# Performance work log

Measured on AMD Instinct MI355X. Metric: run time of the kernel, lower is better.

Reference implementation:

```python
import jax, jax.numpy as jnp
import numpy as np

BATCH = 4096  # number of rows in the sparse input matrix (static for segment_sum)


def setup_inputs() -> dict:
    key = jax.random.key(0)
    k1, k2, k3, k4 = jax.random.split(key, 4)
    nnz = 262144
    in_features, out_features = 32000, 256
    row_idx = jnp.sort(jax.random.randint(k1, (nnz,), 0, BATCH, dtype=jnp.int32))
    col_idx = jax.random.randint(k2, (nnz,), 0, in_features, dtype=jnp.int32)
    vals = jax.random.uniform(k3, (nnz,), dtype=jnp.float32)
    weight = jax.random.normal(k4, (in_features, out_features), dtype=jnp.float32) / np.sqrt(out_features)
    bias = jnp.zeros((out_features,), dtype=jnp.float32)
    return {"row_idx": row_idx, "col_idx": col_idx, "vals": vals,
            "weight": weight, "bias": bias}


def reference(row_idx, col_idx, vals, weight, bias):
    # out = sparse_input @ weight + bias
    # sparse_input is COO: (row_idx, col_idx, vals), shape [BATCH, in_features]
    # gather weight rows for each nonzero, scale by value, sum per output row
    contrib = vals[:, None] * weight[col_idx]          # [nnz, out_features]
    out = jax.ops.segment_sum(contrib, row_idx, num_segments=BATCH)  # [BATCH, out]
    return out + bias
```

## Files before the change

kernel.cpp:

```cpp
#include <hip/hip_runtime.h>


constexpr int BATCH = 4096;
constexpr int ROWS_PER_BLOCK = 4;

__global__ __launch_bounds__(256, 4) void sparse_linear_kernel(
    const int*   __restrict__ row_idx,
    const int*   __restrict__ col_idx,
    const float* __restrict__ vals,
    const float* __restrict__ weight,
    const float* __restrict__ bias,
    float*       __restrict__ out,
    int nnz)
{
    const int wave = threadIdx.x >> 6;
    const int lane = threadIdx.x & 63;
    const int r    = blockIdx.x * ROWS_PER_BLOCK + wave;

    int lo = 0, hi = nnz;
    while (lo < hi) {
        int mid = (lo + hi) >> 1;
        if (row_idx[mid] < r) lo = mid + 1; else hi = mid;
    }
    const int start = lo;
    hi = nnz;
    while (lo < hi) {
        int mid = (lo + hi) >> 1;
        if (row_idx[mid] < r + 1) lo = mid + 1; else hi = mid;
    }
    const int end = lo;

    const float4* __restrict__ W = reinterpret_cast<const float4*>(weight);

    float4 a0 = make_float4(0.f, 0.f, 0.f, 0.f);
    float4 a1 = a0, a2 = a0, a3 = a0;

    int k = start;
    for (; k + 4 <= end; k += 4) {
        const int   c0 = col_idx[k + 0], c1 = col_idx[k + 1];
        const int   c2 = col_idx[k + 2], c3 = col_idx[k + 3];
        const float v0 = vals[k + 0], v1 = vals[k + 1];
        const float v2 = vals[k + 2], v3 = vals[k + 3];
        const float4 w0 = W[(size_t)c0 * 64 + lane];
        const float4 w1 = W[(size_t)c1 * 64 + lane];
        const float4 w2 = W[(size_t)c2 * 64 + lane];
        const float4 w3 = W[(size_t)c3 * 64 + lane];
        a0.x = fmaf(v0, w0.x, a0.x); a0.y = fmaf(v0, w0.y, a0.y);
        a0.z = fmaf(v0, w0.z, a0.z); a0.w = fmaf(v0, w0.w, a0.w);
        a1.x = fmaf(v1, w1.x, a1.x); a1.y = fmaf(v1, w1.y, a1.y);
        a1.z = fmaf(v1, w1.z, a1.z); a1.w = fmaf(v1, w1.w, a1.w);
        a2.x = fmaf(v2, w2.x, a2.x); a2.y = fmaf(v2, w2.y, a2.y);
        a2.z = fmaf(v2, w2.z, a2.z); a2.w = fmaf(v2, w2.w, a2.w);
        a3.x = fmaf(v3, w3.x, a3.x); a3.y = fmaf(v3, w3.y, a3.y);
        a3.z = fmaf(v3, w3.z, a3.z); a3.w = fmaf(v3, w3.w, a3.w);
    }
    for (; k < end; ++k) {
        const int   c = col_idx[k];
        const float v = vals[k];
        const float4 w = W[(size_t)c * 64 + lane];
        a0.x = fmaf(v, w.x, a0.x); a0.y = fmaf(v, w.y, a0.y);
        a0.z = fmaf(v, w.z, a0.z); a0.w = fmaf(v, w.w, a0.w);
    }

    float4 acc;
    acc.x = (a0.x + a1.x) + (a2.x + a3.x);
    acc.y = (a0.y + a1.y) + (a2.y + a3.y);
    acc.z = (a0.z + a1.z) + (a2.z + a3.z);
    acc.w = (a0.w + a1.w) + (a2.w + a3.w);

    const float4 b = reinterpret_cast<const float4*>(bias)[lane];
    float4 o;
    o.x = acc.x + b.x; o.y = acc.y + b.y;
    o.z = acc.z + b.z; o.w = acc.w + b.w;

    reinterpret_cast<float4*>(out)[(size_t)r * 64 + lane] = o;
}

extern "C" void kernel_launch(void* const* d_in, const int* in_sizes, int n_in,
                              void* d_out, int out_size, void* d_ws, size_t ws_size,
                              hipStream_t stream)
{
    const int*   row_idx = (const int*)  d_in[0];
    const int*   col_idx = (const int*)  d_in[1];
    const float* vals    = (const float*)d_in[2];
    const float* weight  = (const float*)d_in[3];
    const float* bias    = (const float*)d_in[4];
    float*       out     = (float*)      d_out;
    const int    nnz     = in_sizes[0];

    dim3 grid(BATCH / ROWS_PER_BLOCK);
    dim3 block(256);
    hipLaunchKernelGGL(sparse_linear_kernel, grid, block, 0, stream,
                       row_idx, col_idx, vals, weight, bias, out, nnz);
}
```

Before: 119.3 us.

## Build CSR row pointers and split each row across four waves

```diff
diff --git a/kernel.cpp b/kernel.cpp
--- a/kernel.cpp
+++ b/kernel.cpp
@@ -2,41 +2,47 @@
 
 
 constexpr int BATCH = 4096;
-constexpr int ROWS_PER_BLOCK = 4;
 
-__global__ __launch_bounds__(256, 4) void sparse_linear_kernel(
-    const int*   __restrict__ row_idx,
+__global__ void build_row_ptr(const int* __restrict__ row_idx, int nnz,
+                              int* __restrict__ ptr)
+{
+    const int i = blockIdx.x * blockDim.x + threadIdx.x;
+    if (i >= nnz) return;
+    const int r  = row_idx[i];
+    const int rn = (i + 1 < nnz) ? row_idx[i + 1] : BATCH;
+    for (int rr = r + 1; rr <= rn; ++rr) ptr[rr] = i + 1;
+    if (i == 0)
+        for (int rr = 0; rr <= r; ++rr) ptr[rr] = 0;
+}
+
+__global__ __launch_bounds__(256, 8) void sparse_linear_kernel(
     const int*   __restrict__ col_idx,
     const float* __restrict__ vals,
     const float* __restrict__ weight,
     const float* __restrict__ bias,
-    float*       __restrict__ out,
-    int nnz)
+    const int*   __restrict__ ptr,
+    float*       __restrict__ out)
 {
+    __shared__ float4 part[4][64];
+
     const int wave = threadIdx.x >> 6;
     const int lane = threadIdx.x & 63;
-    const int r    = blockIdx.x * ROWS_PER_BLOCK + wave;
+    const int r    = blockIdx.x;
 
-    int lo = 0, hi = nnz;
-    while (lo < hi) {
-        int mid = (lo + hi) >> 1;
-        if (row_idx[mid] < r) lo = mid + 1; else hi = mid;
-    }
-    const int start = lo;
-    hi = nnz;
-    while (lo < hi) {
-        int mid = (lo + hi) >> 1;
-        if (row_idx[mid] < r + 1) lo = mid + 1; else hi = mid;
-    }
-    const int end = lo;
+    const int start = ptr[r];
+    const int end   = ptr[r + 1];
+    const int len   = end - start;
+    const int chunk = (len + 3) >> 2;
+
+    int k  = start + wave * chunk;
+    int ke = min(k + chunk, end);
 
     const float4* __restrict__ W = reinterpret_cast<const float4*>(weight);
 
     float4 a0 = make_float4(0.f, 0.f, 0.f, 0.f);
     float4 a1 = a0, a2 = a0, a3 = a0;
 
-    int k = start;
-    for (; k + 4 <= end; k += 4) {
+    for (; k + 4 <= ke; k += 4) {
         const int   c0 = col_idx[k + 0], c1 = col_idx[k + 1];
         const int   c2 = col_idx[k + 2], c3 = col_idx[k + 3];
         const float v0 = vals[k + 0], v1 = vals[k + 1];
@@ -54,7 +60,7 @@
         a3.x = fmaf(v3, w3.x, a3.x); a3.y = fmaf(v3, w3.y, a3.y);
         a3.z = fmaf(v3, w3.z, a3.z); a3.w = fmaf(v3, w3.w, a3.w);
     }
-    for (; k < end; ++k) {
+    for (; k < ke; ++k) {
         const int   c = col_idx[k];
         const float v = vals[k];
         const float4 w = W[(size_t)c * 64 + lane];
@@ -68,12 +74,20 @@
     acc.z = (a0.z + a1.z) + (a2.z + a3.z);
     acc.w = (a0.w + a1.w) + (a2.w + a3.w);
 
-    const float4 b = reinterpret_cast<const float4*>(bias)[lane];
-    float4 o;
-    o.x = acc.x + b.x; o.y = acc.y + b.y;
-    o.z = acc.z + b.z; o.w = acc.w + b.w;
+    part[wave][lane] = acc;
+    __syncthreads();
 
-    reinterpret_cast<float4*>(out)[(size_t)r * 64 + lane] = o;
+    if (wave == 0) {
+        const float4 p0 = part[0][lane], p1 = part[1][lane];
+        const float4 p2 = part[2][lane], p3 = part[3][lane];
+        const float4 b  = reinterpret_cast<const float4*>(bias)[lane];
+        float4 o;
+        o.x = ((p0.x + p1.x) + (p2.x + p3.x)) + b.x;
+        o.y = ((p0.y + p1.y) + (p2.y + p3.y)) + b.y;
+        o.z = ((p0.z + p1.z) + (p2.z + p3.z)) + b.z;
+        o.w = ((p0.w + p1.w) + (p2.w + p3.w)) + b.w;
+        reinterpret_cast<float4*>(out)[(size_t)r * 64 + lane] = o;
+    }
 }
 
 extern "C" void kernel_launch(void* const* d_in, const int* in_sizes, int n_in,
@@ -88,8 +102,10 @@
     float*       out     = (float*)      d_out;
     const int    nnz     = in_sizes[0];
 
-    dim3 grid(BATCH / ROWS_PER_BLOCK);
-    dim3 block(256);
-    hipLaunchKernelGGL(sparse_linear_kernel, grid, block, 0, stream,
-                       row_idx, col_idx, vals, weight, bias, out, nnz);
+    int* row_ptr = (int*)d_ws;
+
+    hipLaunchKernelGGL(build_row_ptr, dim3((nnz + 255) / 256), dim3(256), 0, stream,
+                       row_idx, nnz, row_ptr);
+    hipLaunchKernelGGL(sparse_linear_kernel, dim3(BATCH), dim3(256), 0, stream,
+                       col_idx, vals, weight, bias, row_ptr, out);
 }
```

After: 114.6 us. 1.04x faster.
